# Performance work log

Measured on AMD Instinct MI355X. Metric: run time of the kernel, lower is better.

Reference implementation:

```python
import jax, jax.numpy as jnp
import numpy as np

NUM_HEADS = 32
NUM_KV_HEADS = 8
HEAD_DIM = 128
HIDDEN = 4096
MAX_POS = 4096
ROPE_BASE = 10000.0


def _rope_cache(dtype=jnp.float32):
    inv_freq = 1.0 / (ROPE_BASE ** (jnp.arange(0, HEAD_DIM, 2, dtype=jnp.float32) / HEAD_DIM))
    t = jnp.arange(MAX_POS, dtype=jnp.float32)
    freqs = t[:, None] * inv_freq[None, :]            # [MAX_POS, HEAD_DIM//2]
    emb = jnp.concatenate([freqs, freqs], axis=-1)    # [MAX_POS, HEAD_DIM]
    return jnp.cos(emb).astype(dtype), jnp.sin(emb).astype(dtype)


def _rotate_half(x):
    x1, x2 = jnp.split(x, 2, axis=-1)
    return jnp.concatenate([-x2, x1], axis=-1)


def setup_inputs() -> dict:
    key = jax.random.key(0)
    k1, k2, k3 = jax.random.split(key, 3)
    B, S = 2, 2048
    hidden_states = jax.random.normal(k1, (B, S, HIDDEN), dtype=jnp.float32)
    position_ids = jnp.arange(B * S, dtype=jnp.int64).reshape(B, S) % MAX_POS
    qkv_out = (NUM_HEADS + 2 * NUM_KV_HEADS) * HEAD_DIM  # 6144
    w_qkv = jax.random.normal(k2, (qkv_out, HIDDEN), dtype=jnp.float32) * (HIDDEN ** -0.5)
    w_o = jax.random.normal(k3, (HIDDEN, HIDDEN), dtype=jnp.float32) * (HIDDEN ** -0.5)
    return {"hidden_states": hidden_states, "position_ids": position_ids,
            "w_qkv": w_qkv, "w_o": w_o}


def reference(hidden_states, position_ids, w_qkv, w_o):
    B, S, H = hidden_states.shape
    q_size = NUM_HEADS * HEAD_DIM
    kv_size = NUM_KV_HEADS * HEAD_DIM

    qkv = hidden_states @ w_qkv.T                     # [B,S,6144]
    q, k, v = jnp.split(qkv, [q_size, q_size + kv_size], axis=-1)
    q = q.reshape(B, S, NUM_HEADS, HEAD_DIM).transpose(0, 2, 1, 3)      # [B,Hq,S,D]
    k = k.reshape(B, S, NUM_KV_HEADS, HEAD_DIM).transpose(0, 2, 1, 3)   # [B,Hkv,S,D]
    v = v.reshape(B, S, NUM_KV_HEADS, HEAD_DIM).transpose(0, 2, 1, 3)

    cos_cache, sin_cache = _rope_cache(hidden_states.dtype)
    cos = cos_cache[position_ids][:, None]            # [B,1,S,D]
    sin = sin_cache[position_ids][:, None]
    q = q * cos + _rotate_half(q) * sin
    k = k * cos + _rotate_half(k) * sin

    n_rep = NUM_HEADS // NUM_KV_HEADS
    k = jnp.repeat(k, n_rep, axis=1)                  # [B,Hq,S,D]
    v = jnp.repeat(v, n_rep, axis=1)

    scale = 1.0 / jnp.sqrt(jnp.asarray(HEAD_DIM, hidden_states.dtype))
    scores = jnp.einsum('bhqd,bhkd->bhqk', q, k) * scale
    causal = jnp.tril(jnp.ones((S, S), dtype=bool))
    scores = jnp.where(causal[None, None], scores, jnp.asarray(-1e9, scores.dtype))
    probs = jax.nn.softmax(scores, axis=-1)
    attn = jnp.einsum('bhqk,bhkd->bhqd', probs, v)    # [B,Hq,S,D]
    attn = attn.transpose(0, 2, 1, 3).reshape(B, S, H)
    return attn @ w_o.T
```

## Files before the change

### kernel.cpp

```cpp
#include <hip/hip_runtime.h>


typedef unsigned short u16;
typedef __attribute__((ext_vector_type(8))) short bh8;
typedef __attribute__((ext_vector_type(4))) float f4;

#define MFMA16(a, b, c) __builtin_amdgcn_mfma_f32_16x16x32_bf16(a, b, c, 0, 0, 0)

__device__ __forceinline__ u16 f2bf(float f) {
  union { float f; unsigned u; } v; v.f = f;
  unsigned r = v.u + 0x7fffu + ((v.u >> 16) & 1u);
  return (u16)(r >> 16);
}
__device__ __forceinline__ float bf2f(u16 h) {
  union { unsigned u; float f; } v; v.u = ((unsigned)h) << 16;
  return v.f;
}
__device__ __forceinline__ float rsum16(float v) {
  v += __shfl_xor(v, 1, 64);
  v += __shfl_xor(v, 2, 64);
  v += __shfl_xor(v, 4, 64);
  v += __shfl_xor(v, 8, 64);
  return v;
}

__device__ __forceinline__ bh8 load8_cvt(const float* p) {
  float4 lo = *(const float4*)p;
  float4 hi = *(const float4*)(p + 4);
  bh8 r;
  r[0] = (short)f2bf(lo.x); r[1] = (short)f2bf(lo.y);
  r[2] = (short)f2bf(lo.z); r[3] = (short)f2bf(lo.w);
  r[4] = (short)f2bf(hi.x); r[5] = (short)f2bf(hi.y);
  r[6] = (short)f2bf(hi.z); r[7] = (short)f2bf(hi.w);
  return r;
}
__device__ __forceinline__ bh8 load8_cvt(const u16* p) {
  return *(const bh8*)p;
}
__device__ __forceinline__ void store_c(u16* C, size_t idx, float v) { C[idx] = f2bf(v); }
__device__ __forceinline__ void store_c(float* C, size_t idx, float v) { C[idx] = v; }

__device__ __forceinline__ void gload16(const u16* g, u16* l) {
  __builtin_amdgcn_global_load_lds(
      (const __attribute__((address_space(1))) void*)g,
      (__attribute__((address_space(3))) void*)l, 16, 0, 0);
}

__global__ __launch_bounds__(256) void f32_to_bf16(const float* __restrict__ in,
                                                   u16* __restrict__ out, int n8) {
  int i = blockIdx.x * 256 + threadIdx.x;
  const int stride = gridDim.x * 256;
  for (; i < n8; i += stride) {
    bh8 v = load8_cvt(in + (size_t)i * 8);
    *(bh8*)(out + (size_t)i * 8) = v;
  }
}

template <typename TC>
__global__ __launch_bounds__(256) void gemm_bt_lds(const u16* __restrict__ A,
                                                   const u16* __restrict__ B,
                                                   TC* __restrict__ C,
                                                   int M, int N, int K) {
  __shared__ u16 sA[128 * 32];
  __shared__ u16 sB[128 * 32];
  const int tid = threadIdx.x;
  const int wave = tid >> 6, lane = tid & 63;
  const int quad = lane >> 4, l16 = lane & 15;
  const int bm = blockIdx.y * 128, bn = blockIdx.x * 128;
  const int wm = (wave & 1) * 64, wn = (wave >> 1) * 64;

  f4 zero4 = {0.f, 0.f, 0.f, 0.f};
  f4 acc[4][4];
#pragma unroll
  for (int i = 0; i < 4; i++)
#pragma unroll
    for (int j = 0; j < 4; j++) acc[i][j] = zero4;

  const int ch0 = wave * 2, ch1 = ch0 + 1;
  const int rr = lane >> 2, kc = (lane & 3) * 8;
  const u16* A0 = A + (size_t)(bm + ch0 * 16 + rr) * K + kc;
  const u16* A1 = A + (size_t)(bm + ch1 * 16 + rr) * K + kc;
  const u16* B0 = B + (size_t)(bn + ch0 * 16 + rr) * K + kc;
  const u16* B1 = B + (size_t)(bn + ch1 * 16 + rr) * K + kc;
  u16* la0 = &sA[ch0 * 512];
  u16* la1 = &sA[ch1 * 512];
  u16* lb0 = &sB[ch0 * 512];
  u16* lb1 = &sB[ch1 * 512];

  for (int k0 = 0; k0 < K; k0 += 32) {
    __syncthreads();
    gload16(A0 + k0, la0);
    gload16(A1 + k0, la1);
    gload16(B0 + k0, lb0);
    gload16(B1 + k0, lb1);
    __syncthreads();
    bh8 aF[4], bF[4];
#pragma unroll
    for (int t = 0; t < 4; t++) {
      aF[t] = *(const bh8*)&sA[(wm + t * 16 + l16) * 32 + quad * 8];
      bF[t] = *(const bh8*)&sB[(wn + t * 16 + l16) * 32 + quad * 8];
    }
#pragma unroll
    for (int i = 0; i < 4; i++)
#pragma unroll
      for (int j = 0; j < 4; j++) acc[i][j] = MFMA16(aF[i], bF[j], acc[i][j]);
  }

#pragma unroll
  for (int i = 0; i < 4; i++)
#pragma unroll
    for (int j = 0; j < 4; j++)
#pragma unroll
      for (int r = 0; r < 4; r++) {
        int row = bm + wm + i * 16 + quad * 4 + r;
        int col = bn + wn + j * 16 + l16;
        store_c(C, (size_t)row * N + col, acc[i][j][r]);
      }
}

template <typename TA, typename TB, typename TC>
__global__ __launch_bounds__(256) void gemm_bt(const TA* __restrict__ A,
                                               const TB* __restrict__ B,
                                               TC* __restrict__ C,
                                               int M, int N, int K) {
  __shared__ u16 sA[128 * 32];
  __shared__ u16 sB[128 * 32];
  const int tid = threadIdx.x;
  const int wave = tid >> 6, lane = tid & 63;
  const int quad = lane >> 4, l16 = lane & 15;
  const int bm = blockIdx.y * 128, bn = blockIdx.x * 128;
  const int wm = (wave & 1) * 64, wn = (wave >> 1) * 64;

  f4 zero4 = {0.f, 0.f, 0.f, 0.f};
  f4 acc[4][4];
#pragma unroll
  for (int i = 0; i < 4; i++)
#pragma unroll
    for (int j = 0; j < 4; j++) acc[i][j] = zero4;

  const int c0 = tid, c1 = 256 + tid;
  const TA* Ar0 = A + (size_t)(bm + (c0 >> 2)) * K + (c0 & 3) * 8;
  const TA* Ar1 = A + (size_t)(bm + (c1 >> 2)) * K + (c1 & 3) * 8;
  const TB* Br0 = B + (size_t)(bn + (c0 >> 2)) * K + (c0 & 3) * 8;
  const TB* Br1 = B + (size_t)(bn + (c1 >> 2)) * K + (c1 & 3) * 8;

  for (int k0 = 0; k0 < K; k0 += 32) {
    bh8 a0 = load8_cvt(Ar0 + k0);
    bh8 a1 = load8_cvt(Ar1 + k0);
    bh8 b0 = load8_cvt(Br0 + k0);
    bh8 b1 = load8_cvt(Br1 + k0);
    __syncthreads();
    *(bh8*)&sA[c0 * 8] = a0;
    *(bh8*)&sA[c1 * 8] = a1;
    *(bh8*)&sB[c0 * 8] = b0;
    *(bh8*)&sB[c1 * 8] = b1;
    __syncthreads();
    bh8 aF[4], bF[4];
#pragma unroll
    for (int t = 0; t < 4; t++) {
      aF[t] = *(const bh8*)&sA[(wm + t * 16 + l16) * 32 + quad * 8];
      bF[t] = *(const bh8*)&sB[(wn + t * 16 + l16) * 32 + quad * 8];
    }
#pragma unroll
    for (int i = 0; i < 4; i++)
#pragma unroll
      for (int j = 0; j < 4; j++) acc[i][j] = MFMA16(aF[i], bF[j], acc[i][j]);
  }

#pragma unroll
  for (int i = 0; i < 4; i++)
#pragma unroll
    for (int j = 0; j < 4; j++)
#pragma unroll
      for (int r = 0; r < 4; r++) {
        int row = bm + wm + i * 16 + quad * 4 + r;
        int col = bn + wn + j * 16 + l16;
        store_c(C, (size_t)row * N + col, acc[i][j][r]);
      }
}

__global__ __launch_bounds__(256) void rope_kernel(u16* __restrict__ qkv, const int* __restrict__ pos) {
  __shared__ float cb[64], sb[64];
  const int t = blockIdx.x;
  const int p = pos[t];
  if (threadIdx.x < 64) {
    int j = threadIdx.x;
    float ang = (float)p * exp2f(-0.20762050593046f * (float)j);
    cb[j] = cosf(ang);
    sb[j] = sinf(ang);
  }
  __syncthreads();
  u16* row = qkv + (size_t)t * 6144;
  for (int i = threadIdx.x; i < 2560; i += 256) {
    int head = i >> 6, j = i & 63;
    int off = (head < 32) ? head * 128 : 4096 + (head - 32) * 128;
    float c = cb[j], s = sb[j];
    float x1 = bf2f(row[off + j]);
    float x2 = bf2f(row[off + 64 + j]);
    row[off + j] = f2bf(x1 * c - x2 * s);
    row[off + 64 + j] = f2bf(x2 * c + x1 * s);
  }
}

__global__ __launch_bounds__(256) void v_transpose(const u16* __restrict__ qkv,
                                                   u16* __restrict__ vT) {
  const int b = blockIdx.x;
  const int bbh = b >> 7, d = b & 127;
  const int bb = bbh >> 3, kvh = bbh & 7;
  const int sc = threadIdx.x;
  const u16* src = qkv + (size_t)bb * 2048 * 6144 + 5120 + kvh * 128 + d;
  bh8 r;
#pragma unroll
  for (int j = 0; j < 8; j++) r[j] = (short)src[(size_t)(sc * 8 + j) * 6144];
  *(bh8*)(vT + (size_t)bbh * 128 * 2048 + (size_t)d * 2048 + sc * 8) = r;
}

__global__ __launch_bounds__(256) void attn_fused(const u16* __restrict__ qkv,
                                                  const u16* __restrict__ vT,
                                                  u16* __restrict__ aout) {
  constexpr int LDQ = 6144;
  const int qt = (int)gridDim.y - 1 - (int)blockIdx.y;
  const int bh = blockIdx.x;
  const int bb = bh >> 5, h = bh & 31, kvh = h >> 2;
  const u16* Qb = qkv + (size_t)bb * 2048 * LDQ + h * 128;
  const u16* Kb = qkv + (size_t)bb * 2048 * LDQ + 4096 + kvh * 128;
  const u16* Vt = vT + (size_t)(bb * 8 + kvh) * 128 * 2048;
  u16* Ob = aout + (size_t)bb * 2048 * 4096 + h * 128;

  __shared__ u16 sK[2][64 * 128];
  __shared__ u16 sVT[2][128 * 64];
  __shared__ u16 sP[4][32 * 64];

  const int tid = threadIdx.x;
  const int wave = tid >> 6, lane = tid & 63;
  const int quad = lane >> 4, l16 = lane & 15;
  const int r0 = qt * 128 + wave * 32;

  bh8 qf[2][4];
#pragma unroll
  for (int mt = 0; mt < 2; mt++) {
    int row = r0 + mt * 16 + l16;
#pragma unroll
    for (int kb = 0; kb < 4; kb++)
      qf[mt][kb] = *(const bh8*)(Qb + (size_t)row * LDQ + kb * 32 + quad * 8);
  }

  f4 zero4 = {0.f, 0.f, 0.f, 0.f};
  f4 oacc[2][8];
#pragma unroll
  for (int mt = 0; mt < 2; mt++)
#pragma unroll
    for (int n = 0; n < 8; n++) oacc[mt][n] = zero4;
  float lsum[2][4];
#pragma unroll
  for (int mt = 0; mt < 2; mt++)
#pragma unroll
    for (int r = 0; r < 4; r++) lsum[mt][r] = 0.f;

  const float SCALE = 0.08838834764831845f;
  const float L2E = 1.4426950408889634f;
  const float SC2 = SCALE * L2E;
  const float C0 = 8.0f * L2E;
  const int iters = 2 * qt + 2;
  const int wave_maxrow = r0 + 31;

  const int krin = lane >> 4, kuin = lane & 15;
  const int vrin = lane >> 3, vuin = lane & 7;

  u16* skA = &sK[0][0];  u16* skB = &sK[1][0];
  u16* svA = &sVT[0][0]; u16* svB = &sVT[1][0];
  u16* sPw = &sP[wave][0];

#define STAGE_TILE(SKDST, SVDST, KT)                                          \
  {                                                                           \
    _Pragma("unroll")                                                         \
    for (int i = 0; i < 4; i++) {                                             \
      int c = wave * 4 + i;                                                   \
      int row = c * 4 + krin;                                                 \
      const u16* src = Kb + (size_t)((KT) * 64 + row) * LDQ +                 \
                       ((kuin ^ (row & 7)) << 3);                             \
      gload16(src, (SKDST) + c * 512);                                        \
    }                                                                         \
    _Pragma("unroll")                                                         \
    for (int i = 0; i < 4; i++) {                                             \
      int c = wave * 4 + i;                                                   \
      int d = c * 8 + vrin;                                                   \
      const u16* src = Vt + (size_t)d * 2048 + (KT) * 64 +                    \
                       ((vuin ^ (d & 7)) << 3);                               \
      gload16(src, (SVDST) + c * 512);                                        \
    }                                                                         \
  }

  STAGE_TILE(skA, svA, 0);
  __syncthreads();

  for (int kt = 0; kt < iters; kt++) {
    if (kt + 1 < iters) STAGE_TILE(skB, svB, kt + 1);

    const bool live = (kt * 64 <= wave_maxrow);
    if (live) {
      f4 sc[2][4];
#pragma unroll
      for (int mt = 0; mt < 2; mt++)
#pragma unroll
        for (int nt = 0; nt < 4; nt++) sc[mt][nt] = zero4;
#pragma unroll
      for (int nt = 0; nt < 4; nt++) {
        const int krow = nt * 16 + l16;
        const u16* kp = skA + krow * 128;
        const int sw = krow & 7;
#pragma unroll
        for (int kb = 0; kb < 4; kb++) {
          bh8 kf = *(const bh8*)(kp + (((kb * 4 + quad) ^ sw) << 3));
          sc[0][nt] = MFMA16(qf[0][kb], kf, sc[0][nt]);
          sc[1][nt] = MFMA16(qf[1][kb], kf, sc[1][nt]);
        }
      }
#pragma unroll
      for (int mt = 0; mt < 2; mt++)
#pragma unroll
        for (int nt = 0; nt < 4; nt++)
#pragma unroll
          for (int r = 0; r < 4; r++) {
            int row = r0 + mt * 16 + quad * 4 + r;
            int col = kt * 64 + nt * 16 + l16;
            float p = (col <= row) ? exp2f(sc[mt][nt][r] * SC2 - C0) : 0.f;
            sc[mt][nt][r] = p;
            lsum[mt][r] += p;
          }
#pragma unroll
      for (int mt = 0; mt < 2; mt++)
#pragma unroll
        for (int nt = 0; nt < 4; nt++)
#pragma unroll
          for (int r = 0; r < 4; r++) {
            int prow = mt * 16 + quad * 4 + r;
            int pcol = nt * 16 + l16;
            sPw[prow * 64 + (((pcol >> 3) ^ (prow & 7)) << 3) + (pcol & 7)] =
                f2bf(sc[mt][nt][r]);
          }
      bh8 pf[2][2];
#pragma unroll
      for (int mt = 0; mt < 2; mt++) {
        const int prow = mt * 16 + l16;
        const int sw = prow & 7;
#pragma unroll
        for (int kb2 = 0; kb2 < 2; kb2++)
          pf[mt][kb2] = *(const bh8*)&sPw[prow * 64 + (((kb2 * 4 + quad) ^ sw) << 3)];
      }
#pragma unroll
      for (int n = 0; n < 8; n++) {
        const int vrow = n * 16 + l16;
        const u16* vp = svA + vrow * 64;
        const int sw = vrow & 7;
#pragma unroll
        for (int kb2 = 0; kb2 < 2; kb2++) {
          bh8 vf = *(const bh8*)(vp + (((kb2 * 4 + quad) ^ sw) << 3));
          oacc[0][n] = MFMA16(pf[0][kb2], vf, oacc[0][n]);
          oacc[1][n] = MFMA16(pf[1][kb2], vf, oacc[1][n]);
        }
      }
    }
    __syncthreads();
    u16* t;
    t = skA; skA = skB; skB = t;
    t = svA; svA = svB; svB = t;
  }

#pragma unroll
  for (int mt = 0; mt < 2; mt++) {
    float inv[4];
#pragma unroll
    for (int r = 0; r < 4; r++) inv[r] = 1.0f / rsum16(lsum[mt][r]);
#pragma unroll
    for (int n = 0; n < 8; n++)
#pragma unroll
      for (int r = 0; r < 4; r++) {
        int row = r0 + mt * 16 + quad * 4 + r;
        Ob[(size_t)row * 4096 + n * 16 + l16] = f2bf(oacc[mt][n][r] * inv[r]);
      }
  }
#undef STAGE_TILE
}

extern "C" void kernel_launch(void* const* d_in, const int* in_sizes, int n_in,
                              void* d_out, int out_size, void* d_ws, size_t ws_size,
                              hipStream_t stream) {
  const float* hidden = (const float*)d_in[0];
  const int*   pos    = (const int*)d_in[1];
  const float* w_qkv  = (const float*)d_in[2];
  const float* w_o    = (const float*)d_in[3];
  float* out = (float*)d_out;

  u16* qkv  = (u16*)d_ws;
  u16* aout = (u16*)((char*)d_ws + (size_t)50331648);

  if (ws_size >= (size_t)134217728) {
    u16* hb  = (u16*)((char*)d_ws + (size_t)50331648);
    u16* wqb = (u16*)((char*)d_ws + (size_t)83886080);
    u16* wob = (u16*)((char*)d_ws + (size_t)83886080);
    u16* vT  = (u16*)((char*)d_ws + (size_t)117440512);

    f32_to_bf16<<<dim3(1024), 256, 0, stream>>>(hidden, hb, 2097152);
    f32_to_bf16<<<dim3(1024), 256, 0, stream>>>(w_qkv, wqb, 3145728);
    gemm_bt_lds<u16><<<dim3(48, 32), 256, 0, stream>>>(hb, wqb, qkv, 4096, 6144, 4096);
    f32_to_bf16<<<dim3(1024), 256, 0, stream>>>(w_o, wob, 2097152);
    rope_kernel<<<dim3(4096), 256, 0, stream>>>(qkv, pos);
    v_transpose<<<dim3(2048), 256, 0, stream>>>(qkv, vT);
    attn_fused<<<dim3(64, 16), 256, 0, stream>>>(qkv, vT, aout);
    gemm_bt_lds<float><<<dim3(32, 32), 256, 0, stream>>>(aout, wob, out, 4096, 4096, 4096);
  } else {
    u16* vT = (u16*)((char*)d_ws + (size_t)83886080);
    gemm_bt<float, float, u16><<<dim3(48, 32), 256, 0, stream>>>(
        hidden, w_qkv, qkv, 4096, 6144, 4096);
    rope_kernel<<<dim3(4096), 256, 0, stream>>>(qkv, pos);
    v_transpose<<<dim3(2048), 256, 0, stream>>>(qkv, vT);
    attn_fused<<<dim3(64, 16), 256, 0, stream>>>(qkv, vT, aout);
    gemm_bt<u16, float, float><<<dim3(32, 32), 256, 0, stream>>>(
        aout, w_o, out, 4096, 4096, 4096);
  }
}
```

Measured before the change: 874.9 us.

## Double-buffer GEMM LDS tiles with K=64 stages, XOR swizzle and XCD-aware block mapping

Replaces the single-buffered K=32 LDS GEMM with a double-buffered K=64 pipeline. The next tile's global-to-LDS loads are issued before computing the current one, using an explicit vmcnt wait. LDS columns are XOR-swizzled to avoid bank conflicts, and workgroup IDs are remapped across 8 XCDs to improve L2 locality. This doubles LDS use to 64KB per block, which may reduce occupancy, and the inline waitcnt and barriers are manual scheduling that is easy to get wrong.

Measured after the change: 814.3 us. -6.9%, faster.

```diff
diff --git a/kernel.cpp b/kernel.cpp
--- a/kernel.cpp
+++ b/kernel.cpp
@@ -57,16 +57,22 @@
 }
 
 template <typename TC>
-__global__ __launch_bounds__(256) void gemm_bt_lds(const u16* __restrict__ A,
-                                                   const u16* __restrict__ B,
-                                                   TC* __restrict__ C,
-                                                   int M, int N, int K) {
-  __shared__ u16 sA[128 * 32];
-  __shared__ u16 sB[128 * 32];
+__global__ __launch_bounds__(256) void gemm_bt_p2(const u16* __restrict__ A,
+                                                  const u16* __restrict__ B,
+                                                  TC* __restrict__ C,
+                                                  int M, int N, int K) {
+  __shared__ u16 sA[2][128 * 64];
+  __shared__ u16 sB[2][128 * 64];
   const int tid = threadIdx.x;
   const int wave = tid >> 6, lane = tid & 63;
   const int quad = lane >> 4, l16 = lane & 15;
-  const int bm = blockIdx.y * 128, bn = blockIdx.x * 128;
+
+  const int nbx = gridDim.x;
+  const int nwg = nbx * gridDim.y;
+  const int wg = blockIdx.y * nbx + blockIdx.x;
+  const int cpx = nwg >> 3;
+  const int swz = (wg & 7) * cpx + (wg >> 3);
+  const int bm = (swz / nbx) * 128, bn = (swz % nbx) * 128;
   const int wm = (wave & 1) * 64, wn = (wave >> 1) * 64;
 
   f4 zero4 = {0.f, 0.f, 0.f, 0.f};
@@ -76,34 +82,53 @@
 #pragma unroll
     for (int j = 0; j < 4; j++) acc[i][j] = zero4;
 
-  const int ch0 = wave * 2, ch1 = ch0 + 1;
-  const int rr = lane >> 2, kc = (lane & 3) * 8;
-  const u16* A0 = A + (size_t)(bm + ch0 * 16 + rr) * K + kc;
-  const u16* A1 = A + (size_t)(bm + ch1 * 16 + rr) * K + kc;
-  const u16* B0 = B + (size_t)(bn + ch0 * 16 + rr) * K + kc;
-  const u16* B1 = B + (size_t)(bn + ch1 * 16 + rr) * K + kc;
-  u16* la0 = &sA[ch0 * 512];
-  u16* la1 = &sA[ch1 * 512];
-  u16* lb0 = &sB[ch0 * 512];
-  u16* lb1 = &sB[ch1 * 512];
-
-  for (int k0 = 0; k0 < K; k0 += 32) {
-    __syncthreads();
-    gload16(A0 + k0, la0);
-    gload16(A1 + k0, la1);
-    gload16(B0 + k0, lb0);
-    gload16(B1 + k0, lb1);
-    __syncthreads();
-    bh8 aF[4], bF[4];
-#pragma unroll
-    for (int t = 0; t < 4; t++) {
-      aF[t] = *(const bh8*)&sA[(wm + t * 16 + l16) * 32 + quad * 8];
-      bF[t] = *(const bh8*)&sB[(wn + t * 16 + l16) * 32 + quad * 8];
+  const int srow = lane >> 3, sunit = lane & 7;
+
+#define STAGE_G(KT, SLOT)                                                      \
+  {                                                                            \
+    _Pragma("unroll")                                                          \
+    for (int i = 0; i < 4; i++) {                                              \
+      const int ch = wave * 4 + i;                                             \
+      const int r = ch * 8 + srow;                                             \
+      const int colsw = (KT) * 64 + ((sunit ^ (r & 7)) << 3);                  \
+      gload16(A + (size_t)(bm + r) * K + colsw, &sA[SLOT][ch * 512]);          \
+      gload16(B + (size_t)(bn + r) * K + colsw, &sB[SLOT][ch * 512]);          \
+    }                                                                          \
+  }
+
+  const int NT = K >> 6;
+  STAGE_G(0, 0);
+
+  for (int kt = 0; kt < NT; ++kt) {
+    const int p = kt & 1;
+    if (kt + 1 < NT) {
+      STAGE_G(kt + 1, p ^ 1);
+      asm volatile("s_waitcnt vmcnt(8)" ::: "memory");
+    } else {
+      asm volatile("s_waitcnt vmcnt(0)" ::: "memory");
     }
-#pragma unroll
-    for (int i = 0; i < 4; i++)
-#pragma unroll
-      for (int j = 0; j < 4; j++) acc[i][j] = MFMA16(aF[i], bF[j], acc[i][j]);
+    __builtin_amdgcn_sched_barrier(0);
+    __builtin_amdgcn_s_barrier();
+
+#pragma unroll
+    for (int kb = 0; kb < 2; ++kb) {
+      bh8 aF[4], bF[4];
+#pragma unroll
+      for (int t = 0; t < 4; t++) {
+        const int ra = wm + t * 16 + l16;
+        aF[t] = *(const bh8*)&sA[p][ra * 64 + ((((kb << 2) | quad) ^ (ra & 7)) << 3)];
+        const int rb = wn + t * 16 + l16;
+        bF[t] = *(const bh8*)&sB[p][rb * 64 + ((((kb << 2) | quad) ^ (rb & 7)) << 3)];
+      }
+      __builtin_amdgcn_s_setprio(1);
+#pragma unroll
+      for (int i = 0; i < 4; i++)
+#pragma unroll
+        for (int j = 0; j < 4; j++) acc[i][j] = MFMA16(aF[i], bF[j], acc[i][j]);
+      __builtin_amdgcn_s_setprio(0);
+      if (kb == 0) __builtin_amdgcn_s_barrier();
+    }
+    __builtin_amdgcn_sched_barrier(0);
   }
 
 #pragma unroll
@@ -116,6 +141,7 @@
         int col = bn + wn + j * 16 + l16;
         store_c(C, (size_t)row * N + col, acc[i][j][r]);
       }
+#undef STAGE_G
 }
 
 template <typename TA, typename TB, typename TC>
@@ -403,12 +429,12 @@
 
     f32_to_bf16<<<dim3(1024), 256, 0, stream>>>(hidden, hb, 2097152);
     f32_to_bf16<<<dim3(1024), 256, 0, stream>>>(w_qkv, wqb, 3145728);
-    gemm_bt_lds<u16><<<dim3(48, 32), 256, 0, stream>>>(hb, wqb, qkv, 4096, 6144, 4096);
+    gemm_bt_p2<u16><<<dim3(48, 32), 256, 0, stream>>>(hb, wqb, qkv, 4096, 6144, 4096);
     f32_to_bf16<<<dim3(1024), 256, 0, stream>>>(w_o, wob, 2097152);
     rope_kernel<<<dim3(4096), 256, 0, stream>>>(qkv, pos);
     v_transpose<<<dim3(2048), 256, 0, stream>>>(qkv, vT);
     attn_fused<<<dim3(64, 16), 256, 0, stream>>>(qkv, vT, aout);
-    gemm_bt_lds<float><<<dim3(32, 32), 256, 0, stream>>>(aout, wob, out, 4096, 4096, 4096);
+    gemm_bt_p2<float><<<dim3(32, 32), 256, 0, stream>>>(aout, wob, out, 4096, 4096, 4096);
   } else {
     u16* vT = (u16*)((char*)d_ws + (size_t)83886080);
     gemm_bt<float, float, u16><<<dim3(48, 32), 256, 0, stream>>>(
```
